# Optimization experiments

Measured on AMD Instinct MI355X. Metric: run time of the kernel, lower is better.

## Reference

```python
import jax, jax.numpy as jnp
import numpy as np

B, CIN, COUT, RES, WDIM, K = 16, 512, 512, 64, 512, 3
LRELU_ALPHA = 0.2
ACT_GAIN = float(np.sqrt(2.0))  # bias_act def_gain for lrelu


def setup_inputs() -> dict:
    key = jax.random.key(0)
    ks = jax.random.split(key, 8)
    return {
        "x": jax.random.normal(ks[0], (B, CIN, RES, RES), dtype=jnp.float32),
        "w": jax.random.normal(ks[1], (B, WDIM), dtype=jnp.float32),
        "weight": jax.random.normal(ks[2], (COUT, CIN, K, K), dtype=jnp.float32),
        "bias": jnp.zeros((COUT,), dtype=jnp.float32),
        "affine_w": jax.random.normal(ks[3], (CIN, WDIM), dtype=jnp.float32),
        "affine_b": jnp.ones((CIN,), dtype=jnp.float32),  # bias_init=1
        "noise_const": jax.random.normal(ks[4], (RES, RES), dtype=jnp.float32),
        "noise_strength": jnp.asarray(0.1, dtype=jnp.float32),
    }


def reference(x, w, weight, bias, affine_w, affine_b, noise_const, noise_strength):
    # affine: FullyConnectedLayer with lr-equalized weight scale 1/sqrt(w_dim)
    styles = w @ (affine_w.T * (1.0 / np.sqrt(WDIM))) + affine_b  # [B, CIN]

    # modulate: per-sample scaled weights [B, COUT, CIN, K, K]
    wmod = weight[None] * styles[:, None, :, None, None]
    # demodulate
    demod = jax.lax.rsqrt(jnp.sum(wmod * wmod, axis=(2, 3, 4)) + 1e-8)  # [B, COUT]
    wmod = wmod * demod[:, :, None, None, None]

    # per-sample conv2d, padding=k//2 (StyleGAN2 groups=batch trick -> vmap)
    def conv1(xi, wi):
        return jax.lax.conv_general_dilated(
            xi[None], wi, window_strides=(1, 1),
            padding=[(K // 2, K // 2), (K // 2, K // 2)],
            dimension_numbers=("NCHW", "OIHW", "NCHW"))[0]

    y = jax.vmap(conv1)(x, wmod)  # [B, COUT, RES, RES]

    # noise injection (noise_mode='const'): broadcast [RES,RES] over batch/channel
    y = y + noise_const * noise_strength

    # fused bias + lrelu + gain (conv_clamp=None)
    y = y + bias[None, :, None, None]
    y = jnp.where(y >= 0, y, LRELU_ALPHA * y) * ACT_GAIN
    return y
```

## Files before the change

kernel.cpp:

```cpp
#include <hip/hip_runtime.h>
#include <hip/hip_bf16.h>

#define B_     16
#define CIN_   512
#define COUT_  512
#define RES_   64
#define WDIM_  512
#define LRELU_A 0.2f
#define GAIN_  1.4142135623730951f

typedef __attribute__((ext_vector_type(8)))  __bf16 bf16x8;
typedef __attribute__((ext_vector_type(16))) float  f32x16;
typedef __attribute__((ext_vector_type(4)))  int    int4v;
typedef __attribute__((ext_vector_type(8)))  unsigned short u16x8;

__device__ __forceinline__ unsigned short f2bf(float f) {
    union { float f; unsigned int u; } v; v.f = f;
    unsigned int u = v.u;
    return (unsigned short)((u + 0x7FFFu + ((u >> 16) & 1u)) >> 16);
}

__device__ __forceinline__ void gl_lds16(const void* g, void* l) {
    __builtin_amdgcn_global_load_lds(
        (const __attribute__((address_space(1))) unsigned int*)g,
        (__attribute__((address_space(3))) unsigned int*)l, 16, 0, 0);
}

__global__ void styles_k(const float* __restrict__ w, const float* __restrict__ aw,
                         const float* __restrict__ ab, float* __restrict__ styles) {
    int idx = blockIdx.x * 256 + threadIdx.x;
    int b = idx >> 9, ci = idx & 511;
    const float4* wp = (const float4*)(w + b * WDIM_);
    const float4* ap = (const float4*)(aw + (size_t)ci * WDIM_);
    float acc = 0.f;
    #pragma unroll 4
    for (int k = 0; k < WDIM_ / 4; ++k) {
        float4 a = ap[k], q = wp[k];
        acc += a.x * q.x + a.y * q.y + a.z * q.z + a.w * q.w;
    }
    styles[idx] = acc * 0.04419417382415922f + ab[ci];
}

__global__ void wprep_k(const float* __restrict__ weight, unsigned short* __restrict__ wt,
                        float* __restrict__ wsq) {
    int idx = blockIdx.x * 256 + threadIdx.x;
    int co = idx >> 9, ci = idx & 511;
    const float* wp = weight + (size_t)idx * 9;
    float s = 0.f;
    #pragma unroll
    for (int t = 0; t < 9; ++t) {
        float f = wp[t];
        s += f * f;
        wt[(((size_t)(ci >> 4) * 9 + t) * 512 + co) * 16 + (ci & 15)] = f2bf(f);
    }
    wsq[idx] = s;
}

__global__ void demod_k(const float* __restrict__ styles, const float* __restrict__ wsq,
                        float* __restrict__ demod) {
    int idx = blockIdx.x * 256 + threadIdx.x;
    int b = idx >> 9, co = idx & 511;
    const float4* wr = (const float4*)(wsq + (size_t)co * CIN_);
    const float4* sr = (const float4*)(styles + (size_t)b * CIN_);
    float acc = 0.f;
    #pragma unroll 4
    for (int ci = 0; ci < CIN_ / 4; ++ci) {
        float4 q = wr[ci], s = sr[ci];
        acc += q.x * s.x * s.x + q.y * s.y * s.y + q.z * s.z * s.z + q.w * s.w * s.w;
    }
    demod[idx] = rsqrtf(acc + 1e-8f);
}

__global__ void xprep_k(const float* __restrict__ x, const float* __restrict__ styles,
                        unsigned short* __restrict__ xs) {
    __shared__ float tile[64][65];
    __shared__ float styv[64];
    int bid = blockIdx.x;
    int ct = bid & 7, rr = (bid >> 3) % 66, b = bid / 528;
    int tid = threadIdx.x;
    unsigned short* xo = xs + (size_t)(b * 66 + rr) * 32768 + (size_t)ct * 4096;
    if (rr == 0 || rr == 65) {
        u16x8 z = {0, 0, 0, 0, 0, 0, 0, 0};
        #pragma unroll
        for (int it = 0; it < 2; ++it) {
            int s = it * 256 + tid;
            int ccl = s >> 7, w = (s >> 1) & 63, half = s & 1;
            *(u16x8*)(xo + ccl * 1024 + w * 16 + half * 8) = z;
        }
        return;
    }
    int h = rr - 1;
    if (tid < 64) styv[tid] = styles[b * CIN_ + ct * 64 + tid];
    const float* xp = x + (((size_t)(b * CIN_ + ct * 64)) * RES_ + h) * RES_;
    #pragma unroll
    for (int it = 0; it < 4; ++it) {
        int ci = it * 16 + (tid >> 4);
        int w4 = (tid & 15) * 4;
        float4 v = *(const float4*)(xp + (size_t)ci * (RES_ * RES_) + w4);
        tile[ci][w4] = v.x; tile[ci][w4 + 1] = v.y; tile[ci][w4 + 2] = v.z; tile[ci][w4 + 3] = v.w;
    }
    __syncthreads();
    #pragma unroll
    for (int it = 0; it < 2; ++it) {
        int s = it * 256 + tid;
        int ccl = s >> 7, w = (s >> 1) & 63, half = s & 1;
        int ci0 = ccl * 16 + half * 8;
        u16x8 v;
        #pragma unroll
        for (int j = 0; j < 8; ++j) v[j] = f2bf(tile[ci0 + j][w] * styv[ci0 + j]);
        *(u16x8*)(xo + ccl * 1024 + w * 16 + half * 8) = v;
    }
}

#define XBUF 12672

#define LOADAF(PH, CC, DY) do {                                              \
    const char* p_ = wb_ + (size_t)((CC) * 9 + (DY) * 3) * 16384;            \
    _Pragma("unroll") for (int tt_ = 0; tt_ < 3; ++tt_)                      \
      _Pragma("unroll") for (int mt_ = 0; mt_ < 2; ++mt_)                    \
        af[PH][tt_][mt_] = *(const bf16x8*)(p_ + tt_ * 16384 + mt_ * 1024);  \
  } while (0)

#define PHASE(CC, DY, PH, NPH, NCC, NDY, GUARD) do {                         \
    const char* Xb = Xl + ((CC) & 1) * XBUF;                                 \
    bf16x8 bv[3][4];                                                         \
    _Pragma("unroll") for (int tt_ = 0; tt_ < 3; ++tt_)                      \
      _Pragma("unroll") for (int nt_ = 0; nt_ < 4; ++nt_) {                  \
        int o_ = (((nt_ & 1) * 32) + l31 + tt_) * 32 + (kg << 4);            \
        bv[tt_][nt_] = *(const bf16x8*)(Xb + (rp * 2 + (nt_ >> 1) + (DY)) * 2112 + o_); \
      }                                                                      \
    if (GUARD) { LOADAF(NPH, NCC, NDY); }                                    \
    __builtin_amdgcn_s_setprio(1);                                           \
    _Pragma("unroll") for (int tt_ = 0; tt_ < 3; ++tt_)                      \
      _Pragma("unroll") for (int mt_ = 0; mt_ < 2; ++mt_)                    \
        _Pragma("unroll") for (int nt_ = 0; nt_ < 4; ++nt_)                  \
          acc[mt_][nt_] = __builtin_amdgcn_mfma_f32_32x32x16_bf16(           \
              af[PH][tt_][mt_], bv[tt_][nt_], acc[mt_][nt_], 0, 0, 0);       \
    __builtin_amdgcn_s_setprio(0);                                           \
  } while (0)

__global__ __launch_bounds__(256, 2) void conv_k(
    const unsigned short* __restrict__ xs, const unsigned short* __restrict__ wt,
    const float* __restrict__ demod, const float* __restrict__ bias,
    const float* __restrict__ noise, const float* __restrict__ nsp,
    float* __restrict__ out)
{
    __shared__ __align__(16) char Xl[2 * XBUF];

    const int tid  = threadIdx.x;
    const int lane = tid & 63;
    const int wid  = tid >> 6;
    const int l31  = lane & 31;
    const int kg   = lane >> 5;
    const int ch   = wid & 1;
    const int rp   = wid >> 1;

    const int lb = ((blockIdx.x & 7) << 7) | (blockIdx.x >> 3);
    const int m  = lb >> 8;
    const int rest = lb & 255;
    const int b  = rest >> 4;
    const int h0 = (rest & 15) * 4;

    if (tid < 48) {
        int buf = tid / 24, rem = tid % 24, r = rem >> 2, k = rem & 3;
        int chunk = r * 132 + (k < 2 ? k : 128 + k);
        int4v z = {0, 0, 0, 0};
        *(int4v*)(Xl + buf * XBUF + chunk * 16) = z;
    }

    const char* xsrc = (const char*)xs + (size_t)(b * 66 + h0) * 65536;
    auto stageX = [&](int cc, int buf) {
        const char* s0 = xsrc + cc * 2048;
        char* d0 = Xl + buf * XBUF;
        #pragma unroll
        for (int k = 0; k < 3; ++k) {
            const int c0 = k * 256 + (wid << 6);
            const int r  = c0 >> 7;
            gl_lds16(s0 + (size_t)r * 65536 + (size_t)((c0 + lane) & 127) * 16,
                     d0 + (r * 132 + ((c0 & 127) + 2)) * 16);
        }
    };

    const char* wb_ = (const char*)wt
        + (size_t)((m * 128 + ch * 64 + l31) * 32 + kg * 16);

    f32x16 acc[2][4];
    #pragma unroll
    for (int mt = 0; mt < 2; ++mt)
        #pragma unroll
        for (int nt = 0; nt < 4; ++nt)
            #pragma unroll
            for (int j = 0; j < 16; ++j) acc[mt][nt][j] = 0.f;

    bf16x8 af[2][3][2];

    stageX(0, 0);
    LOADAF(0, 0, 0);
    __syncthreads();

    for (int pb = 0; pb < 16; ++pb) {
        const int ccE = pb * 2, ccO = ccE + 1;
        stageX(ccO, 1);
        PHASE(ccE, 0, 0, 1, ccE, 1, true);
        PHASE(ccE, 1, 1, 0, ccE, 2, true);
        PHASE(ccE, 2, 0, 1, ccO, 0, true);
        __syncthreads();
        if (pb < 15) stageX(ccO + 1, 0);
        PHASE(ccO, 0, 1, 0, ccO, 1, true);
        PHASE(ccO, 1, 0, 1, ccO, 2, true);
        PHASE(ccO, 2, 1, 0, ccO + 1, 0, (pb < 15));
        if (pb < 15) __syncthreads();
    }

    const float nsv = nsp[0];
    float nz[4];
    #pragma unroll
    for (int nt = 0; nt < 4; ++nt)
        nz[nt] = noise[(h0 + rp * 2 + (nt >> 1)) * 64 + (nt & 1) * 32 + l31] * nsv;
    #pragma unroll
    for (int mt = 0; mt < 2; ++mt) {
        #pragma unroll
        for (int j = 0; j < 16; ++j) {
            int co = m * 128 + ch * 64 + mt * 32 + (j & 3) + 8 * (j >> 2) + 4 * kg;
            float d  = demod[b * COUT_ + co];
            float bs = bias[co];
            #pragma unroll
            for (int nt = 0; nt < 4; ++nt) {
                int h = h0 + rp * 2 + (nt >> 1);
                int w = (nt & 1) * 32 + l31;
                float v = acc[mt][nt][j] * d + nz[nt] + bs;
                v = (v >= 0.f ? v : LRELU_A * v) * GAIN_;
                out[((size_t)(b * COUT_ + co) * RES_ + h) * RES_ + w] = v;
            }
        }
    }
}

extern "C" void kernel_launch(void* const* d_in, const int* in_sizes, int n_in,
                              void* d_out, int out_size, void* d_ws, size_t ws_size,
                              hipStream_t stream) {
    const float* x    = (const float*)d_in[0];
    const float* w    = (const float*)d_in[1];
    const float* wgt  = (const float*)d_in[2];
    const float* bias = (const float*)d_in[3];
    const float* aw   = (const float*)d_in[4];
    const float* ab   = (const float*)d_in[5];
    const float* noi  = (const float*)d_in[6];
    const float* ns   = (const float*)d_in[7];
    float* out = (float*)d_out;

    char* ws = (char*)d_ws;
    float* styles        = (float*)(ws);
    float* demod         = (float*)(ws + 32768);
    float* wsq           = (float*)(ws + 65536);
    unsigned short* wt   = (unsigned short*)(ws + 1114112);
    unsigned short* xs   = (unsigned short*)(ws + 6291456);

    hipLaunchKernelGGL(styles_k, dim3(32),   dim3(256), 0, stream, w, aw, ab, styles);
    hipLaunchKernelGGL(xprep_k,  dim3(8448), dim3(256), 0, stream, x, styles, xs);
    hipLaunchKernelGGL(wprep_k,  dim3(1024), dim3(256), 0, stream, wgt, wt, wsq);
    hipLaunchKernelGGL(demod_k,  dim3(32),   dim3(256), 0, stream, styles, wsq, demod);
    hipLaunchKernelGGL(conv_k,   dim3(1024), dim3(256), 0, stream,
                       xs, wt, demod, bias, noi, ns, out);
}
```

Baseline: 536.5 us.

## Interleave X staging into phases with partial vmcnt barriers, split weight prep

The conv main loop now issues the next X tile's global-to-LDS loads inside the first phase of each half. Full __syncthreads are replaced by s_waitcnt vmcnt(6) plus s_barrier, so the prefetched A-fragment loads can stay in flight across the barrier. The weight prep is split into a coalesced-write transpose kernel and a separate sum-of-squares kernel. xprep stores its LDS tile with float4 writes using padded rows. The hand-counted vmcnt value is fragile: if the compiler reorders or changes the number of outstanding loads, the barrier could wait on too few and let the X buffer be read before it is filled.

Measured after the change: 557.5 us. +3.9%, slower.

```diff
diff --git a/kernel.cpp b/kernel.cpp
--- a/kernel.cpp
+++ b/kernel.cpp
@@ -41,18 +41,27 @@
     styles[idx] = acc * 0.04419417382415922f + ab[ci];
 }
 
-__global__ void wprep_k(const float* __restrict__ weight, unsigned short* __restrict__ wt,
-                        float* __restrict__ wsq) {
+__global__ void wprep_wt(const float* __restrict__ weight, unsigned short* __restrict__ wt) {
+    int blk = blockIdx.x;
+    int cc = blk / 9, t = blk % 9;
+    int co = threadIdx.x;
+    const float* wp = weight + ((size_t)co * 512 + cc * 16) * 9 + t;
+    u16x8 lo, hi;
+    #pragma unroll
+    for (int j = 0; j < 8; ++j) lo[j] = f2bf(wp[j * 9]);
+    #pragma unroll
+    for (int j = 0; j < 8; ++j) hi[j] = f2bf(wp[(j + 8) * 9]);
+    unsigned short* o = wt + (((size_t)cc * 9 + t) * 512 + co) * 16;
+    *(u16x8*)o = lo;
+    *(u16x8*)(o + 8) = hi;
+}
+
+__global__ void wsq_k(const float* __restrict__ weight, float* __restrict__ wsq) {
     int idx = blockIdx.x * 256 + threadIdx.x;
-    int co = idx >> 9, ci = idx & 511;
     const float* wp = weight + (size_t)idx * 9;
     float s = 0.f;
     #pragma unroll
-    for (int t = 0; t < 9; ++t) {
-        float f = wp[t];
-        s += f * f;
-        wt[(((size_t)(ci >> 4) * 9 + t) * 512 + co) * 16 + (ci & 15)] = f2bf(f);
-    }
+    for (int t = 0; t < 9; ++t) { float f = wp[t]; s += f * f; }
     wsq[idx] = s;
 }
 
@@ -73,7 +82,7 @@
 
 __global__ void xprep_k(const float* __restrict__ x, const float* __restrict__ styles,
                         unsigned short* __restrict__ xs) {
-    __shared__ float tile[64][65];
+    __shared__ float tile[64][68];
     __shared__ float styv[64];
     int bid = blockIdx.x;
     int ct = bid & 7, rr = (bid >> 3) % 66, b = bid / 528;
@@ -97,7 +106,7 @@
         int ci = it * 16 + (tid >> 4);
         int w4 = (tid & 15) * 4;
         float4 v = *(const float4*)(xp + (size_t)ci * (RES_ * RES_) + w4);
-        tile[ci][w4] = v.x; tile[ci][w4 + 1] = v.y; tile[ci][w4 + 2] = v.z; tile[ci][w4 + 3] = v.w;
+        *(float4*)&tile[ci][w4] = v;
     }
     __syncthreads();
     #pragma unroll
@@ -114,28 +123,35 @@
 
 #define XBUF 12672
 
-#define LOADAF(PH, CC, DY) do {                                              \
+#define LOADAF(SLOT, CC, DY) do {                                            \
     const char* p_ = wb_ + (size_t)((CC) * 9 + (DY) * 3) * 16384;            \
     _Pragma("unroll") for (int tt_ = 0; tt_ < 3; ++tt_)                      \
       _Pragma("unroll") for (int mt_ = 0; mt_ < 2; ++mt_)                    \
-        af[PH][tt_][mt_] = *(const bf16x8*)(p_ + tt_ * 16384 + mt_ * 1024);  \
+        af[SLOT][tt_][mt_] = *(const bf16x8*)(p_ + tt_ * 16384 + mt_ * 1024);\
   } while (0)
 
-#define PHASE(CC, DY, PH, NPH, NCC, NDY, GUARD) do {                         \
-    const char* Xb = Xl + ((CC) & 1) * XBUF;                                 \
+#define BARRIER6() do {                                                      \
+    asm volatile("s_waitcnt vmcnt(6)" ::: "memory");                         \
+    __builtin_amdgcn_s_barrier();                                            \
+    __builtin_amdgcn_sched_barrier(0);                                       \
+  } while (0)
+
+#define PHASE(CC, DY, SLOT, LG, LSLOT, LCC, LDY, XG, XCC, XBI) do {          \
+    const char* Xb_ = Xl + ((CC) & 1) * XBUF;                                \
     bf16x8 bv[3][4];                                                         \
     _Pragma("unroll") for (int tt_ = 0; tt_ < 3; ++tt_)                      \
       _Pragma("unroll") for (int nt_ = 0; nt_ < 4; ++nt_) {                  \
         int o_ = (((nt_ & 1) * 32) + l31 + tt_) * 32 + (kg << 4);            \
-        bv[tt_][nt_] = *(const bf16x8*)(Xb + (rp * 2 + (nt_ >> 1) + (DY)) * 2112 + o_); \
+        bv[tt_][nt_] = *(const bf16x8*)(Xb_ + (rp * 2 + (nt_ >> 1) + (DY)) * 2112 + o_); \
       }                                                                      \
-    if (GUARD) { LOADAF(NPH, NCC, NDY); }                                    \
+    if (LG) { LOADAF(LSLOT, LCC, LDY); }                                     \
+    if (XG) { stageX(XCC, XBI); }                                            \
     __builtin_amdgcn_s_setprio(1);                                           \
     _Pragma("unroll") for (int tt_ = 0; tt_ < 3; ++tt_)                      \
       _Pragma("unroll") for (int mt_ = 0; mt_ < 2; ++mt_)                    \
         _Pragma("unroll") for (int nt_ = 0; nt_ < 4; ++nt_)                  \
           acc[mt_][nt_] = __builtin_amdgcn_mfma_f32_32x32x16_bf16(           \
-              af[PH][tt_][mt_], bv[tt_][nt_], acc[mt_][nt_], 0, 0, 0);       \
+              af[SLOT][tt_][mt_], bv[tt_][nt_], acc[mt_][nt_], 0, 0, 0);     \
     __builtin_amdgcn_s_setprio(0);                                           \
   } while (0)
 
@@ -196,20 +212,21 @@
 
     stageX(0, 0);
     LOADAF(0, 0, 0);
-    __syncthreads();
+    asm volatile("s_waitcnt vmcnt(6) lgkmcnt(0)" ::: "memory");
+    __builtin_amdgcn_s_barrier();
+    __builtin_amdgcn_sched_barrier(0);
 
     for (int pb = 0; pb < 16; ++pb) {
         const int ccE = pb * 2, ccO = ccE + 1;
-        stageX(ccO, 1);
-        PHASE(ccE, 0, 0, 1, ccE, 1, true);
-        PHASE(ccE, 1, 1, 0, ccE, 2, true);
-        PHASE(ccE, 2, 0, 1, ccO, 0, true);
-        __syncthreads();
-        if (pb < 15) stageX(ccO + 1, 0);
-        PHASE(ccO, 0, 1, 0, ccO, 1, true);
-        PHASE(ccO, 1, 0, 1, ccO, 2, true);
-        PHASE(ccO, 2, 1, 0, ccO + 1, 0, (pb < 15));
-        if (pb < 15) __syncthreads();
+        const bool nx = (pb < 15);
+        PHASE(ccE,  0, 0,   true, 1,   ccE,    1,   true,   ccO,    1);
+        PHASE(ccE,  1, 1,   true, 0,   ccE,    2,   false,  0,      0);
+        PHASE(ccE,  2, 0,   true, 1,   ccO,    0,   false,  0,      0);
+        BARRIER6();
+        PHASE(ccO,  0, 1,   true, 0,   ccO,    1,   nx,     ccE+2,  0);
+        PHASE(ccO,  1, 0,   true, 1,   ccO,    2,   false,  0,      0);
+        PHASE(ccO,  2, 1,   nx,   0,   ccE+2,  0,   false,  0,      0);
+        if (nx) BARRIER6();
     }
 
     const float nsv = nsp[0];
@@ -257,8 +274,9 @@
     unsigned short* xs   = (unsigned short*)(ws + 6291456);
 
     hipLaunchKernelGGL(styles_k, dim3(32),   dim3(256), 0, stream, w, aw, ab, styles);
+    hipLaunchKernelGGL(wprep_wt, dim3(288),  dim3(512), 0, stream, wgt, wt);
+    hipLaunchKernelGGL(wsq_k,    dim3(1024), dim3(256), 0, stream, wgt, wsq);
     hipLaunchKernelGGL(xprep_k,  dim3(8448), dim3(256), 0, stream, x, styles, xs);
-    hipLaunchKernelGGL(wprep_k,  dim3(1024), dim3(256), 0, stream, wgt, wt, wsq);
     hipLaunchKernelGGL(demod_k,  dim3(32),   dim3(256), 0, stream, styles, wsq, demod);
     hipLaunchKernelGGL(conv_k,   dim3(1024), dim3(256), 0, stream,
                        xs, wt, demod, bias, noi, ns, out);
```
